# Kernel optimization log

Measured on AMD Instinct MI355X. Metric: run time of the kernel, lower is better.

Reference implementation:

```python
import jax, jax.numpy as jnp
from jax import lax
import numpy as np

V, C, L, H, TCTX = 50257, 768, 12, 12, 1024
B, T = 2, 1024
HD = C // H


def setup_inputs() -> dict:
    key = jax.random.key(0)
    ks = jax.random.split(key, 18)
    std = 0.02
    std_proj = 0.02 * (2 * L) ** -0.5  # SCALE_INIT residual projections
    n = lambda k, shape, s: (jax.random.normal(k, shape, jnp.float32) * s)
    return {
        "idx": jax.random.randint(ks[0], (B, T), 0, V),
        "wte": n(ks[1], (V, C), std),            # tied with lm_head
        "wpe": n(ks[2], (TCTX, C), std),
        "ln1_w": jnp.ones((L, C), jnp.float32),
        "ln1_b": jnp.zeros((L, C), jnp.float32),
        "attn_w": n(ks[3], (L, C, 3 * C), std),
        "attn_b": jnp.zeros((L, 3 * C), jnp.float32),
        "proj_w": n(ks[4], (L, C, C), std_proj),
        "proj_b": jnp.zeros((L, C), jnp.float32),
        "ln2_w": jnp.ones((L, C), jnp.float32),
        "ln2_b": jnp.zeros((L, C), jnp.float32),
        "fc_w": n(ks[5], (L, C, 4 * C), std),
        "fc_b": jnp.zeros((L, 4 * C), jnp.float32),
        "fcp_w": n(ks[6], (L, 4 * C, C), std_proj),
        "fcp_b": jnp.zeros((L, C), jnp.float32),
        "lnf_w": jnp.ones((C,), jnp.float32),
        "lnf_b": jnp.zeros((C,), jnp.float32),
    }


def _ln(x, w, b, eps=1e-5):
    m = jnp.mean(x, -1, keepdims=True)
    v = jnp.var(x, -1, keepdims=True)
    return (x - m) * lax.rsqrt(v + eps) * w + b


def _gpt_forward(idx, wte, wpe, ln1_w, ln1_b, attn_w, attn_b, proj_w, proj_b,
                 ln2_w, ln2_b, fc_w, fc_b, fcp_w, fcp_b, lnf_w, lnf_b):
    b, t = idx.shape
    x = wte[idx] + wpe[:t]                       # (B,T,C)
    causal = jnp.tril(jnp.ones((t, t), bool))    # (T,T)
    scale = HD ** -0.5

    def block(x, p):
        l1w, l1b, aw, ab, pw, pb, l2w, l2b, fw, fb, fpw, fpb = p
        h = _ln(x, l1w, l1b)
        qkv = h @ aw + ab                        # (B,T,3C)
        q, k, v = jnp.split(qkv, 3, axis=-1)
        q = q.reshape(b, t, H, HD)
        k = k.reshape(b, t, H, HD)
        v = v.reshape(b, t, H, HD)
        att = jnp.einsum('bqhd,bkhd->bhqk', q, k) * scale
        att = jnp.where(causal, att, -jnp.inf)
        att = jax.nn.softmax(att, axis=-1)
        y = jnp.einsum('bhqk,bkhd->bqhd', att, v).reshape(b, t, C)
        x = x + y @ pw + pb
        h2 = _ln(x, l2w, l2b)
        x = x + jax.nn.gelu(h2 @ fw + fb, approximate=True) @ fpw + fpb
        return x, None

    x, _ = lax.scan(block, x, (ln1_w, ln1_b, attn_w, attn_b, proj_w, proj_b,
                               ln2_w, ln2_b, fc_w, fc_b, fcp_w, fcp_b))
    x = _ln(x, lnf_w, lnf_b)
    return x @ wte.T                             # tied lm_head, (B,T,V)


def reference(idx, wte, wpe, ln1_w, ln1_b, attn_w, attn_b, proj_w, proj_b,
              ln2_w, ln2_b, fc_w, fc_b, fcp_w, fcp_b, lnf_w, lnf_b):
    return _gpt_forward(idx, wte, wpe, ln1_w, ln1_b, attn_w, attn_b, proj_w,
                        proj_b, ln2_w, ln2_b, fc_w, fc_b, fcp_w, fcp_b,
                        lnf_w, lnf_b)
```

## Files before the change

kernel.cpp:

```cpp
#include <hip/hip_runtime.h>
#include <math.h>

#define VV 50257
#define CC 768
#define LL 12
#define HH 12
#define TT 1024
#define BB 2
#define BT 2048
#define HD 64

typedef unsigned short u16;
using bf8 = __attribute__((ext_vector_type(8))) short;
using f32x4 = __attribute__((ext_vector_type(4))) float;

__device__ __forceinline__ u16 bf16_rne(float f) {
    unsigned u = __float_as_uint(f);
    unsigned r = u + 0x7FFF + ((u >> 16) & 1);
    return (u16)(r >> 16);
}
__device__ __forceinline__ float bf16_tof(u16 s) {
    return __uint_as_float(((unsigned)s) << 16);
}
__device__ __forceinline__ void split2(float f, u16& h, u16& l) {
    h = bf16_rne(f);
    l = bf16_rne(f - bf16_tof(h));
}
__device__ __forceinline__ float gelu_f(float u) {
    return 0.5f * u * (1.f + tanhf(0.7978845608f * (u + 0.044715f * u * u * u)));
}
__device__ __forceinline__ float wave_sum(float v) {
#pragma unroll
    for (int off = 1; off < 64; off <<= 1) v += __shfl_xor(v, off, 64);
    return v;
}
__device__ __forceinline__ float wave_max(float v) {
#pragma unroll
    for (int off = 1; off < 64; off <<= 1) v = fmaxf(v, __shfl_xor(v, off, 64));
    return v;
}

__global__ __launch_bounds__(256) void embed_k(const int* __restrict__ idx,
                                               const float* __restrict__ wte,
                                               const float* __restrict__ wpe,
                                               float* __restrict__ x) {
    int row = blockIdx.x;
    int t = row & (TT - 1);
    long tok = idx[row];
    const float* a = wte + tok * (long)CC;
    const float* p = wpe + (long)t * CC;
    float* d = x + (long)row * CC;
    for (int c = threadIdx.x; c < CC; c += 256) d[c] = a[c] + p[c];
}

__global__ __launch_bounds__(256) void ln_k(const float* __restrict__ in,
                                            const float* __restrict__ w,
                                            const float* __restrict__ b,
                                            u16* __restrict__ oh, u16* __restrict__ ol) {
    int row = blockIdx.x;
    const float* src = in + (long)row * CC;
    float v[3];
    float s = 0.f, sq = 0.f;
#pragma unroll
    for (int i = 0; i < 3; i++) {
        v[i] = src[threadIdx.x + 256 * i];
        s += v[i];
        sq += v[i] * v[i];
    }
    s = wave_sum(s);
    sq = wave_sum(sq);
    __shared__ float ls[4], lq[4];
    int wid = threadIdx.x >> 6, lane = threadIdx.x & 63;
    if (lane == 0) { ls[wid] = s; lq[wid] = sq; }
    __syncthreads();
    s = ls[0] + ls[1] + ls[2] + ls[3];
    sq = lq[0] + lq[1] + lq[2] + lq[3];
    float mean = s * (1.f / CC);
    float var = sq * (1.f / CC) - mean * mean;
    float rstd = rsqrtf(var + 1e-5f);
#pragma unroll
    for (int i = 0; i < 3; i++) {
        int c = threadIdx.x + 256 * i;
        float val = (v[i] - mean) * rstd * w[c] + b[c];
        u16 hh, lo;
        split2(val, hh, lo);
        oh[(long)row * CC + c] = hh;
        ol[(long)row * CC + c] = lo;
    }
}

__global__ __launch_bounds__(256) void tsplit(const float* __restrict__ W,
                                              u16* __restrict__ Dh,
                                              int K, int N, long wstride, long ostride) {
    __shared__ float tile[16][65];
    int t = threadIdx.x;
    int k0 = blockIdx.y * 16, n0 = blockIdx.x * 64;
    const float* src = W + (long)blockIdx.z * wstride;
    u16* dh = Dh + (long)blockIdx.z * ostride;
    u16* dl = dh + (long)K * N;
    {
        int k = t >> 4, n4 = (t & 15) * 4;
        float4 v = *(const float4*)&src[(long)(k0 + k) * N + n0 + n4];
        tile[k][n4] = v.x; tile[k][n4 + 1] = v.y; tile[k][n4 + 2] = v.z; tile[k][n4 + 3] = v.w;
    }
    __syncthreads();
    int n = t >> 2, kq = (t & 3) * 4;
    u16 h[4], l[4];
#pragma unroll
    for (int j = 0; j < 4; j++) split2(tile[kq + j][n], h[j], l[j]);
    long off = (long)(n0 + n) * K + k0 + kq;
    *(uint2*)&dh[off] = make_uint2((unsigned)h[0] | ((unsigned)h[1] << 16),
                                   (unsigned)h[2] | ((unsigned)h[3] << 16));
    *(uint2*)&dl[off] = make_uint2((unsigned)l[0] | ((unsigned)l[1] << 16),
                                   (unsigned)l[2] | ((unsigned)l[3] << 16));
}

template <int EPI>
__global__ __launch_bounds__(256, 2) void gemm_mfma(
    const u16* __restrict__ Ah, const u16* __restrict__ Al,
    const u16* __restrict__ Bh, const u16* __restrict__ Bl,
    const float* __restrict__ bias, const float* __restrict__ res,
    float* __restrict__ outf, u16* __restrict__ oh, u16* __restrict__ ol,
    int N, int K) {
    __shared__ u16 lds[16][1040];
    int tid = threadIdx.x, lane = tid & 63, wid = tid >> 6;
    long bm = (long)blockIdx.y * 128, bn = (long)blockIdx.x * 128;
    const u16* srcs[4] = {Ah + bm * K, Al + bm * K, Bh + bn * K, Bl + bn * K};
    f32x4 acc[4][4];
#pragma unroll
    for (int i = 0; i < 4; i++)
#pragma unroll
        for (int j = 0; j < 4; j++) acc[i][j] = (f32x4){0.f, 0.f, 0.f, 0.f};
    int wr = (wid >> 1) * 64, wc = (wid & 1) * 64;
    int lrow = lane & 15, lkg = lane >> 4;

    for (int k0 = 0; k0 < K; k0 += 32) {
#pragma unroll
        for (int mat = 0; mat < 4; mat++)
#pragma unroll
            for (int i = 0; i < 2; i++) {
                int slot = tid + 256 * i;
                int row = slot >> 2, kg = slot & 3;
                int4 v = *(const int4*)(srcs[mat] + (long)row * K + k0 + kg * 8);
                *(int4*)&lds[mat * 4 + kg][row * 8] = v;
            }
        __syncthreads();
        bf8 ah[4], al[4], bh[4], bl[4];
#pragma unroll
        for (int m = 0; m < 4; m++) {
            ah[m] = *(const bf8*)&lds[0 + lkg][(wr + m * 16 + lrow) * 8];
            al[m] = *(const bf8*)&lds[4 + lkg][(wr + m * 16 + lrow) * 8];
            bh[m] = *(const bf8*)&lds[8 + lkg][(wc + m * 16 + lrow) * 8];
            bl[m] = *(const bf8*)&lds[12 + lkg][(wc + m * 16 + lrow) * 8];
        }
#pragma unroll
        for (int m = 0; m < 4; m++)
#pragma unroll
            for (int n = 0; n < 4; n++) {
                acc[m][n] = __builtin_amdgcn_mfma_f32_16x16x32_bf16(al[m], bh[n], acc[m][n], 0, 0, 0);
                acc[m][n] = __builtin_amdgcn_mfma_f32_16x16x32_bf16(ah[m], bl[n], acc[m][n], 0, 0, 0);
                acc[m][n] = __builtin_amdgcn_mfma_f32_16x16x32_bf16(ah[m], bh[n], acc[m][n], 0, 0, 0);
            }
        __syncthreads();
    }
#pragma unroll
    for (int m = 0; m < 4; m++)
#pragma unroll
        for (int n = 0; n < 4; n++)
#pragma unroll
            for (int r = 0; r < 4; r++) {
                long row = bm + wr + m * 16 + (lane >> 4) * 4 + r;
                long col = bn + wc + n * 16 + (lane & 15);
                float v = acc[m][n][r] + bias[col];
                long off = row * N + col;
                if (EPI == 0) outf[off] = v;
                if (EPI == 1) outf[off] = v + res[off];
                if (EPI == 2) {
                    float g = gelu_f(v);
                    u16 hh, lo;
                    split2(g, hh, lo);
                    oh[off] = hh;
                    ol[off] = lo;
                }
            }
}

__global__ __launch_bounds__(256, 2) void gemm_lmh(const u16* __restrict__ Ah,
                                                   const u16* __restrict__ Al,
                                                   const float* __restrict__ W,
                                                   float* __restrict__ outf) {
    __shared__ u16 lds[16][1040];
    int tid = threadIdx.x, lane = tid & 63, wid = tid >> 6;
    long bm = (long)blockIdx.y * 128, bn = (long)blockIdx.x * 128;
    const int K = CC;
    const u16* srcs[2] = {Ah + bm * K, Al + bm * K};
    f32x4 acc[4][4];
#pragma unroll
    for (int i = 0; i < 4; i++)
#pragma unroll
        for (int j = 0; j < 4; j++) acc[i][j] = (f32x4){0.f, 0.f, 0.f, 0.f};
    int wr = (wid >> 1) * 64, wc = (wid & 1) * 64;
    int lrow = lane & 15, lkg = lane >> 4;

    for (int k0 = 0; k0 < K; k0 += 32) {
#pragma unroll
        for (int mat = 0; mat < 2; mat++)
#pragma unroll
            for (int i = 0; i < 2; i++) {
                int slot = tid + 256 * i;
                int row = slot >> 2, kg = slot & 3;
                int4 v = *(const int4*)(srcs[mat] + (long)row * K + k0 + kg * 8);
                *(int4*)&lds[mat * 4 + kg][row * 8] = v;
            }
#pragma unroll
        for (int i = 0; i < 4; i++) {
            int f = tid + 256 * i;
            int row = f >> 3, c4 = f & 7;
            long srow = bn + row;
            if (srow >= VV) srow = VV - 1;
            float4 v = *(const float4*)&W[srow * (long)CC + k0 + c4 * 4];
            u16 h0, l0, h1, l1, h2, l2, h3, l3;
            split2(v.x, h0, l0); split2(v.y, h1, l1);
            split2(v.z, h2, l2); split2(v.w, h3, l3);
            int kg = c4 >> 1, jo = (c4 & 1) * 4;
            *(uint2*)&lds[8 + kg][row * 8 + jo] =
                make_uint2((unsigned)h0 | ((unsigned)h1 << 16), (unsigned)h2 | ((unsigned)h3 << 16));
            *(uint2*)&lds[12 + kg][row * 8 + jo] =
                make_uint2((unsigned)l0 | ((unsigned)l1 << 16), (unsigned)l2 | ((unsigned)l3 << 16));
        }
        __syncthreads();
        bf8 ah[4], al[4], bh[4], bl[4];
#pragma unroll
        for (int m = 0; m < 4; m++) {
            ah[m] = *(const bf8*)&lds[0 + lkg][(wr + m * 16 + lrow) * 8];
            al[m] = *(const bf8*)&lds[4 + lkg][(wr + m * 16 + lrow) * 8];
            bh[m] = *(const bf8*)&lds[8 + lkg][(wc + m * 16 + lrow) * 8];
            bl[m] = *(const bf8*)&lds[12 + lkg][(wc + m * 16 + lrow) * 8];
        }
#pragma unroll
        for (int m = 0; m < 4; m++)
#pragma unroll
            for (int n = 0; n < 4; n++) {
                acc[m][n] = __builtin_amdgcn_mfma_f32_16x16x32_bf16(al[m], bh[n], acc[m][n], 0, 0, 0);
                acc[m][n] = __builtin_amdgcn_mfma_f32_16x16x32_bf16(ah[m], bl[n], acc[m][n], 0, 0, 0);
                acc[m][n] = __builtin_amdgcn_mfma_f32_16x16x32_bf16(ah[m], bh[n], acc[m][n], 0, 0, 0);
            }
        __syncthreads();
    }
#pragma unroll
    for (int m = 0; m < 4; m++)
#pragma unroll
        for (int n = 0; n < 4; n++)
#pragma unroll
            for (int r = 0; r < 4; r++) {
                long row = bm + wr + m * 16 + (lane >> 4) * 4 + r;
                long col = bn + wc + n * 16 + (lane & 15);
                if (col < VV) outf[row * (long)VV + col] = acc[m][n][r];
            }
}

__global__ __launch_bounds__(256) void attn2(const float* __restrict__ qkv,
                                             u16* __restrict__ yh, u16* __restrict__ yl) {
    __shared__ float qs[16][65], Kt[64][65], Vt[64][65], ps[4][4][64];
    int tid = threadIdx.x, lane = tid & 63, wid = tid >> 6;
    int bh = blockIdx.x >> 6, qg = blockIdx.x & 63;
    int b = bh / HH, hh = bh % HH;
    int qbase = qg * 16;
    const float* base = qkv + (long)b * TT * 3 * CC + hh * HD;
    {
        int r = tid >> 4, d4 = (tid & 15) * 4;
        float4 v = *(const float4*)&base[(long)(qbase + r) * (3 * CC) + d4];
        qs[r][d4] = v.x; qs[r][d4 + 1] = v.y; qs[r][d4 + 2] = v.z; qs[r][d4 + 3] = v.w;
    }
    float o[4] = {0.f, 0.f, 0.f, 0.f};
    float mm[4] = {-INFINITY, -INFINITY, -INFINITY, -INFINITY};
    float sden[4] = {0.f, 0.f, 0.f, 0.f};
    int r0 = qbase + wid * 4;
    for (int k0 = 0; k0 <= qbase + 15; k0 += 64) {
        __syncthreads();
#pragma unroll
        for (int i = 0; i < 8; i++) {
            int f = tid + 256 * i;
            int kk = (f >> 4) & 63, d4 = (f & 15) * 4, isv = f >> 10;
            float4 v = *(const float4*)&base[(long)(k0 + kk) * (3 * CC) + CC + isv * CC + d4];
            float* dst = isv ? &Vt[kk][d4] : &Kt[kk][d4];
            dst[0] = v.x; dst[1] = v.y; dst[2] = v.z; dst[3] = v.w;
        }
        __syncthreads();
        float s[4] = {0.f, 0.f, 0.f, 0.f};
#pragma unroll 16
        for (int d = 0; d < 64; d++) {
            float kd = Kt[lane][d];
#pragma unroll
            for (int i = 0; i < 4; i++) s[i] = fmaf(qs[wid * 4 + i][d], kd, s[i]);
        }
#pragma unroll
        for (int i = 0; i < 4; i++) {
            int qrow = r0 + i;
            bool ok = (k0 + lane) <= qrow;
            float sc = ok ? s[i] * 0.125f : -INFINITY;
            float nm = fmaxf(mm[i], wave_max(sc));
            float p = ok ? expf(sc - nm) : 0.f;
            float ts = wave_sum(p);
            float rs = expf(mm[i] - nm);
            sden[i] = sden[i] * rs + ts;
            o[i] *= rs;
            mm[i] = nm;
            ps[wid][i][lane] = p;
        }
#pragma unroll 16
        for (int kk = 0; kk < 64; kk++) {
            float vv = Vt[kk][lane];
#pragma unroll
            for (int i = 0; i < 4; i++) o[i] = fmaf(ps[wid][i][kk], vv, o[i]);
        }
    }
#pragma unroll
    for (int i = 0; i < 4; i++) {
        float val = o[i] / sden[i];
        long off = (long)(b * TT + r0 + i) * CC + hh * HD + lane;
        u16 hi, lo;
        split2(val, hi, lo);
        yh[off] = hi;
        yl[off] = lo;
    }
}

extern "C" void kernel_launch(void* const* d_in, const int* in_sizes, int n_in,
                              void* d_out, int out_size, void* d_ws, size_t ws_size,
                              hipStream_t stream) {
    const int* idx = (const int*)d_in[0];
    const float* wte = (const float*)d_in[1];
    const float* wpe = (const float*)d_in[2];
    const float* ln1_w = (const float*)d_in[3];
    const float* ln1_b = (const float*)d_in[4];
    const float* attn_w = (const float*)d_in[5];
    const float* attn_b = (const float*)d_in[6];
    const float* proj_w = (const float*)d_in[7];
    const float* proj_b = (const float*)d_in[8];
    const float* ln2_w = (const float*)d_in[9];
    const float* ln2_b = (const float*)d_in[10];
    const float* fc_w = (const float*)d_in[11];
    const float* fc_b = (const float*)d_in[12];
    const float* fcp_w = (const float*)d_in[13];
    const float* fcp_b = (const float*)d_in[14];
    const float* lnf_w = (const float*)d_in[15];
    const float* lnf_b = (const float*)d_in[16];
    float* out = (float*)d_out;

    const long WB_LAYER = 14155776;
    const size_t wb_bytes = (size_t)LL * WB_LAYER * 2;
    char* out_end = (char*)d_out + (size_t)out_size * 4;
    u16* wb = (u16*)(out_end - wb_bytes);

    size_t h_plane = (size_t)BT * CC * 2;
    size_t x_b = (size_t)BT * CC * 4;
    size_t ff_plane = (size_t)BT * 4 * CC * 2;
    size_t qkv_b = (size_t)BT * 3 * CC * 4;
    size_t act_rest = x_b + 2 * ff_plane + qkv_b;
    u16* h_hi = (u16*)d_ws;
    u16* h_lo = h_hi + (size_t)BT * CC;
    char* rest = (ws_size >= 2 * h_plane + act_rest) ? ((char*)d_ws + 2 * h_plane)
                                                     : ((char*)wb - act_rest);
    float* x = (float*)rest;
    u16* ff_hi = (u16*)(rest + x_b);
    u16* ff_lo = ff_hi + (size_t)BT * 4 * CC;
    float* qkvb = (float*)(rest + x_b + 2 * ff_plane);

    tsplit<<<dim3(36, 48, 12), 256, 0, stream>>>(attn_w, wb + 0, CC, 3 * CC, (long)CC * 3 * CC, WB_LAYER);
    tsplit<<<dim3(12, 48, 12), 256, 0, stream>>>(proj_w, wb + 3538944, CC, CC, (long)CC * CC, WB_LAYER);
    tsplit<<<dim3(48, 48, 12), 256, 0, stream>>>(fc_w, wb + 4718592, CC, 4 * CC, (long)CC * 4 * CC, WB_LAYER);
    tsplit<<<dim3(12, 192, 12), 256, 0, stream>>>(fcp_w, wb + 9437184, 4 * CC, CC, (long)4 * CC * CC, WB_LAYER);

    embed_k<<<BT, 256, 0, stream>>>(idx, wte, wpe, x);

    for (int l = 0; l < LL; l++) {
        u16* wl = wb + (long)l * WB_LAYER;
        u16 *aw_h = wl, *aw_l = wl + 1769472;
        u16 *pw_h = wl + 3538944, *pw_l = pw_h + 589824;
        u16 *fw_h = wl + 4718592, *fw_l = fw_h + 2359296;
        u16 *qw_h = wl + 9437184, *qw_l = qw_h + 2359296;

        ln_k<<<BT, 256, 0, stream>>>(x, ln1_w + l * CC, ln1_b + l * CC, h_hi, h_lo);
        gemm_mfma<0><<<dim3(18, 16), 256, 0, stream>>>(h_hi, h_lo, aw_h, aw_l,
            attn_b + (long)l * 3 * CC, nullptr, qkvb, nullptr, nullptr, 3 * CC, CC);
        attn2<<<BB * HH * 64, 256, 0, stream>>>(qkvb, h_hi, h_lo);
        gemm_mfma<1><<<dim3(6, 16), 256, 0, stream>>>(h_hi, h_lo, pw_h, pw_l,
            proj_b + (long)l * CC, x, x, nullptr, nullptr, CC, CC);
        ln_k<<<BT, 256, 0, stream>>>(x, ln2_w + l * CC, ln2_b + l * CC, h_hi, h_lo);
        gemm_mfma<2><<<dim3(24, 16), 256, 0, stream>>>(h_hi, h_lo, fw_h, fw_l,
            fc_b + (long)l * 4 * CC, nullptr, nullptr, ff_hi, ff_lo, 4 * CC, CC);
        gemm_mfma<1><<<dim3(6, 16), 256, 0, stream>>>(ff_hi, ff_lo, qw_h, qw_l,
            fcp_b + (long)l * CC, x, x, nullptr, nullptr, CC, 4 * CC);
    }

    ln_k<<<BT, 256, 0, stream>>>(x, lnf_w, lnf_b, h_hi, h_lo);
    gemm_lmh<<<dim3(393, 16), 256, 0, stream>>>(h_hi, h_lo, wte, out);
}
```

Measured before the change: 7.437 ms.

## Use direct global-to-LDS loads with swizzled LDS layout in MFMA GEMMs

The GEMM tile loads now use global_load_lds to write straight into LDS instead of staging through registers, and the LDS tile moves to a row-major layout with an XOR swizzle to avoid bank conflicts. B fragments are now loaded per column block inside the MFMA loop, which lowers register pressure, and launch bounds go from 2 to 3 blocks per CU. The grid order is swapped so consecutive blocks share the same weight tile, and the LM head gets an XCD-aware block remap for L2 locality. The risks are that the swizzle indexing must exactly match the lane-to-address pattern of global_load_lds, and that the higher occupancy target may cause register spills.

```diff
diff --git a/kernel.cpp b/kernel.cpp
--- a/kernel.cpp
+++ b/kernel.cpp
@@ -38,6 +38,12 @@
 #pragma unroll
     for (int off = 1; off < 64; off <<= 1) v = fmaxf(v, __shfl_xor(v, off, 64));
     return v;
+}
+
+__device__ __forceinline__ void gload16(const void* gsrc, void* ldst) {
+    __builtin_amdgcn_global_load_lds(
+        (const __attribute__((address_space(1))) void*)gsrc,
+        (__attribute__((address_space(3))) void*)ldst, 16, 0, 0);
 }
 
 __global__ __launch_bounds__(256) void embed_k(const int* __restrict__ idx,
@@ -116,15 +122,15 @@
 }
 
 template <int EPI>
-__global__ __launch_bounds__(256, 2) void gemm_mfma(
+__global__ __launch_bounds__(256, 3) void gemm_mfma(
     const u16* __restrict__ Ah, const u16* __restrict__ Al,
     const u16* __restrict__ Bh, const u16* __restrict__ Bl,
     const float* __restrict__ bias, const float* __restrict__ res,
     float* __restrict__ outf, u16* __restrict__ oh, u16* __restrict__ ol,
     int N, int K) {
-    __shared__ u16 lds[16][1040];
+    __shared__ __attribute__((aligned(16))) u16 lds[4][4096];
     int tid = threadIdx.x, lane = tid & 63, wid = tid >> 6;
-    long bm = (long)blockIdx.y * 128, bn = (long)blockIdx.x * 128;
+    long bm = (long)blockIdx.x * 128, bn = (long)blockIdx.y * 128;
     const u16* srcs[4] = {Ah + bm * K, Al + bm * K, Bh + bn * K, Bl + bn * K};
     f32x4 acc[4][4];
 #pragma unroll
@@ -134,33 +140,41 @@
     int wr = (wid >> 1) * 64, wc = (wid & 1) * 64;
     int lrow = lane & 15, lkg = lane >> 4;
 
+    int slot0 = wid * 64 + lane;
+    int row0 = slot0 >> 2, sk0 = (slot0 & 3) ^ ((row0 >> 1) & 3);
+    int slot1 = slot0 + 256;
+    int row1 = slot1 >> 2, sk1 = (slot1 & 3) ^ ((row1 >> 1) & 3);
+    char* lbase0 = (char*)&lds[0][0] + wid * 1024;
+    char* lbase1 = lbase0 + 4096;
+
     for (int k0 = 0; k0 < K; k0 += 32) {
 #pragma unroll
-        for (int mat = 0; mat < 4; mat++)
-#pragma unroll
-            for (int i = 0; i < 2; i++) {
-                int slot = tid + 256 * i;
-                int row = slot >> 2, kg = slot & 3;
-                int4 v = *(const int4*)(srcs[mat] + (long)row * K + k0 + kg * 8);
-                *(int4*)&lds[mat * 4 + kg][row * 8] = v;
+        for (int mat = 0; mat < 4; mat++) {
+            gload16(srcs[mat] + (long)row0 * K + k0 + sk0 * 8, lbase0 + mat * 8192);
+            gload16(srcs[mat] + (long)row1 * K + k0 + sk1 * 8, lbase1 + mat * 8192);
+        }
+        __syncthreads();
+        bf8 ah[4], al[4];
+#pragma unroll
+        for (int m = 0; m < 4; m++) {
+            int r = wr + m * 16 + lrow;
+            int off = r * 32 + ((lkg ^ ((r >> 1) & 3)) * 8);
+            ah[m] = *(const bf8*)&lds[0][off];
+            al[m] = *(const bf8*)&lds[1][off];
+        }
+#pragma unroll
+        for (int n = 0; n < 4; n++) {
+            int r = wc + n * 16 + lrow;
+            int off = r * 32 + ((lkg ^ ((r >> 1) & 3)) * 8);
+            bf8 bh = *(const bf8*)&lds[2][off];
+            bf8 bl = *(const bf8*)&lds[3][off];
+#pragma unroll
+            for (int m = 0; m < 4; m++) {
+                acc[m][n] = __builtin_amdgcn_mfma_f32_16x16x32_bf16(al[m], bh, acc[m][n], 0, 0, 0);
+                acc[m][n] = __builtin_amdgcn_mfma_f32_16x16x32_bf16(ah[m], bl, acc[m][n], 0, 0, 0);
+                acc[m][n] = __builtin_amdgcn_mfma_f32_16x16x32_bf16(ah[m], bh, acc[m][n], 0, 0, 0);
             }
-        __syncthreads();
-        bf8 ah[4], al[4], bh[4], bl[4];
-#pragma unroll
-        for (int m = 0; m < 4; m++) {
-            ah[m] = *(const bf8*)&lds[0 + lkg][(wr + m * 16 + lrow) * 8];
-            al[m] = *(const bf8*)&lds[4 + lkg][(wr + m * 16 + lrow) * 8];
-            bh[m] = *(const bf8*)&lds[8 + lkg][(wc + m * 16 + lrow) * 8];
-            bl[m] = *(const bf8*)&lds[12 + lkg][(wc + m * 16 + lrow) * 8];
-        }
-#pragma unroll
-        for (int m = 0; m < 4; m++)
-#pragma unroll
-            for (int n = 0; n < 4; n++) {
-                acc[m][n] = __builtin_amdgcn_mfma_f32_16x16x32_bf16(al[m], bh[n], acc[m][n], 0, 0, 0);
-                acc[m][n] = __builtin_amdgcn_mfma_f32_16x16x32_bf16(ah[m], bl[n], acc[m][n], 0, 0, 0);
-                acc[m][n] = __builtin_amdgcn_mfma_f32_16x16x32_bf16(ah[m], bh[n], acc[m][n], 0, 0, 0);
-            }
+        }
         __syncthreads();
     }
 #pragma unroll
@@ -185,13 +199,17 @@
             }
 }
 
-__global__ __launch_bounds__(256, 2) void gemm_lmh(const u16* __restrict__ Ah,
+__global__ __launch_bounds__(256, 3) void gemm_lmh(const u16* __restrict__ Ah,
                                                    const u16* __restrict__ Al,
                                                    const float* __restrict__ W,
                                                    float* __restrict__ outf) {
-    __shared__ u16 lds[16][1040];
+    __shared__ __attribute__((aligned(16))) u16 lds[4][4096];
     int tid = threadIdx.x, lane = tid & 63, wid = tid >> 6;
-    long bm = (long)blockIdx.y * 128, bn = (long)blockIdx.x * 128;
+    const int NWG8 = (16 * 393) >> 3;
+    int bid = blockIdx.x;
+    int wg = (bid & 7) * NWG8 + (bid >> 3);
+    long bm = (long)(wg & 15) * 128;
+    long bn = (long)(wg >> 4) * 128;
     const int K = CC;
     const u16* srcs[2] = {Ah + bm * K, Al + bm * K};
     f32x4 acc[4][4];
@@ -202,16 +220,19 @@
     int wr = (wid >> 1) * 64, wc = (wid & 1) * 64;
     int lrow = lane & 15, lkg = lane >> 4;
 
+    int slot0 = wid * 64 + lane;
+    int row0 = slot0 >> 2, sk0 = (slot0 & 3) ^ ((row0 >> 1) & 3);
+    int slot1 = slot0 + 256;
+    int row1 = slot1 >> 2, sk1 = (slot1 & 3) ^ ((row1 >> 1) & 3);
+    char* lbase0 = (char*)&lds[0][0] + wid * 1024;
+    char* lbase1 = lbase0 + 4096;
+
     for (int k0 = 0; k0 < K; k0 += 32) {
 #pragma unroll
-        for (int mat = 0; mat < 2; mat++)
-#pragma unroll
-            for (int i = 0; i < 2; i++) {
-                int slot = tid + 256 * i;
-                int row = slot >> 2, kg = slot & 3;
-                int4 v = *(const int4*)(srcs[mat] + (long)row * K + k0 + kg * 8);
-                *(int4*)&lds[mat * 4 + kg][row * 8] = v;
-            }
+        for (int mat = 0; mat < 2; mat++) {
+            gload16(srcs[mat] + (long)row0 * K + k0 + sk0 * 8, lbase0 + mat * 8192);
+            gload16(srcs[mat] + (long)row1 * K + k0 + sk1 * 8, lbase1 + mat * 8192);
+        }
 #pragma unroll
         for (int i = 0; i < 4; i++) {
             int f = tid + 256 * i;
@@ -222,29 +243,35 @@
             u16 h0, l0, h1, l1, h2, l2, h3, l3;
             split2(v.x, h0, l0); split2(v.y, h1, l1);
             split2(v.z, h2, l2); split2(v.w, h3, l3);
-            int kg = c4 >> 1, jo = (c4 & 1) * 4;
-            *(uint2*)&lds[8 + kg][row * 8 + jo] =
+            int g = c4 >> 1;
+            int boff = row * 64 + ((g ^ ((row >> 1) & 3)) * 16) + (c4 & 1) * 8;
+            *(uint2*)((char*)&lds[2][0] + boff) =
                 make_uint2((unsigned)h0 | ((unsigned)h1 << 16), (unsigned)h2 | ((unsigned)h3 << 16));
-            *(uint2*)&lds[12 + kg][row * 8 + jo] =
+            *(uint2*)((char*)&lds[3][0] + boff) =
                 make_uint2((unsigned)l0 | ((unsigned)l1 << 16), (unsigned)l2 | ((unsigned)l3 << 16));
         }
         __syncthreads();
-        bf8 ah[4], al[4], bh[4], bl[4];
+        bf8 ah[4], al[4];
 #pragma unroll
         for (int m = 0; m < 4; m++) {
-            ah[m] = *(const bf8*)&lds[0 + lkg][(wr + m * 16 + lrow) * 8];
-            al[m] = *(const bf8*)&lds[4 + lkg][(wr + m * 16 + lrow) * 8];
-            bh[m] = *(const bf8*)&lds[8 + lkg][(wc + m * 16 + lrow) * 8];
-            bl[m] = *(const bf8*)&lds[12 + lkg][(wc + m * 16 + lrow) * 8];
-        }
-#pragma unroll
-        for (int m = 0; m < 4; m++)
-#pragma unroll
-            for (int n = 0; n < 4; n++) {
-                acc[m][n] = __builtin_amdgcn_mfma_f32_16x16x32_bf16(al[m], bh[n], acc[m][n], 0, 0, 0);
-                acc[m][n] = __builtin_amdgcn_mfma_f32_16x16x32_bf16(ah[m], bl[n], acc[m][n], 0, 0, 0);
-                acc[m][n] = __builtin_amdgcn_mfma_f32_16x16x32_bf16(ah[m], bh[n], acc[m][n], 0, 0, 0);
+            int r = wr + m * 16 + lrow;
+            int off = r * 32 + ((lkg ^ ((r >> 1) & 3)) * 8);
+            ah[m] = *(const bf8*)&lds[0][off];
+            al[m] = *(const bf8*)&lds[1][off];
+        }
+#pragma unroll
+        for (int n = 0; n < 4; n++) {
+            int r = wc + n * 16 + lrow;
+            int off = r * 32 + ((lkg ^ ((r >> 1) & 3)) * 8);
+            bf8 bh = *(const bf8*)&lds[2][off];
+            bf8 bl = *(const bf8*)&lds[3][off];
+#pragma unroll
+            for (int m = 0; m < 4; m++) {
+                acc[m][n] = __builtin_amdgcn_mfma_f32_16x16x32_bf16(al[m], bh, acc[m][n], 0, 0, 0);
+                acc[m][n] = __builtin_amdgcn_mfma_f32_16x16x32_bf16(ah[m], bl, acc[m][n], 0, 0, 0);
+                acc[m][n] = __builtin_amdgcn_mfma_f32_16x16x32_bf16(ah[m], bh, acc[m][n], 0, 0, 0);
             }
+        }
         __syncthreads();
     }
 #pragma unroll
@@ -382,18 +409,18 @@
         u16 *qw_h = wl + 9437184, *qw_l = qw_h + 2359296;
 
         ln_k<<<BT, 256, 0, stream>>>(x, ln1_w + l * CC, ln1_b + l * CC, h_hi, h_lo);
-        gemm_mfma<0><<<dim3(18, 16), 256, 0, stream>>>(h_hi, h_lo, aw_h, aw_l,
+        gemm_mfma<0><<<dim3(16, 18), 256, 0, stream>>>(h_hi, h_lo, aw_h, aw_l,
             attn_b + (long)l * 3 * CC, nullptr, qkvb, nullptr, nullptr, 3 * CC, CC);
         attn2<<<BB * HH * 64, 256, 0, stream>>>(qkvb, h_hi, h_lo);
-        gemm_mfma<1><<<dim3(6, 16), 256, 0, stream>>>(h_hi, h_lo, pw_h, pw_l,
+        gemm_mfma<1><<<dim3(16, 6), 256, 0, stream>>>(h_hi, h_lo, pw_h, pw_l,
             proj_b + (long)l * CC, x, x, nullptr, nullptr, CC, CC);
         ln_k<<<BT, 256, 0, stream>>>(x, ln2_w + l * CC, ln2_b + l * CC, h_hi, h_lo);
-        gemm_mfma<2><<<dim3(24, 16), 256, 0, stream>>>(h_hi, h_lo, fw_h, fw_l,
+        gemm_mfma<2><<<dim3(16, 24), 256, 0, stream>>>(h_hi, h_lo, fw_h, fw_l,
             fc_b + (long)l * 4 * CC, nullptr, nullptr, ff_hi, ff_lo, 4 * CC, CC);
-        gemm_mfma<1><<<dim3(6, 16), 256, 0, stream>>>(ff_hi, ff_lo, qw_h, qw_l,
+        gemm_mfma<1><<<dim3(16, 6), 256, 0, stream>>>(ff_hi, ff_lo, qw_h, qw_l,
             fcp_b + (long)l * CC, x, x, nullptr, nullptr, CC, 4 * CC);
     }
 
     ln_k<<<BT, 256, 0, stream>>>(x, lnf_w, lnf_b, h_hi, h_lo);
-    gemm_lmh<<<dim3(393, 16), 256, 0, stream>>>(h_hi, h_lo, wte, out);
-}
+    gemm_lmh<<<dim3(16 * 393), 256, 0, stream>>>(h_hi, h_lo, wte, out);
+}
```

Result: faster. 7.187 ms (-3.4%).
